# Optimization experiments

Hardware: AMD Instinct MI355X
Metric: run time of the kernel (lower is better)

Reference implementation:

```python
import jax, jax.numpy as jnp
import numpy as np

D_MODEL = 512
N_HEADS = 8
DH = D_MODEL // N_HEADS


def _split_heads(x, h):
    B, L, D = x.shape
    return x.reshape(B, L, h, D // h).transpose(0, 2, 1, 3)  # [B,h,L,Dh]


def setup_inputs() -> dict:
    key = jax.random.key(0)
    ks = jax.random.split(key, 10)
    B, La, Lb, Lc = 4, 256, 256, 32
    s = 1.0 / np.sqrt(D_MODEL)
    return {
        "Q_in": jax.random.normal(ks[0], (B, La, D_MODEL), jnp.float32),
        "K_in": jax.random.normal(ks[1], (B, Lb, D_MODEL), jnp.float32),
        "V_in": jax.random.normal(ks[2], (B, Lb, D_MODEL), jnp.float32),
        "C_tokens": jax.random.normal(ks[3], (B, Lc, D_MODEL), jnp.float32),
        "Wq": jax.random.normal(ks[4], (D_MODEL, D_MODEL), jnp.float32) * s,
        "bq": jnp.zeros((D_MODEL,), jnp.float32),
        "Wk": jax.random.normal(ks[5], (D_MODEL, D_MODEL), jnp.float32) * s,
        "bk": jnp.zeros((D_MODEL,), jnp.float32),
        "Wv": jax.random.normal(ks[6], (D_MODEL, D_MODEL), jnp.float32) * s,
        "bv": jnp.zeros((D_MODEL,), jnp.float32),
    }


def reference(Q_in, K_in, V_in, C_tokens, Wq, bq, Wk, bk, Wv, bv):
    B, La, D = Q_in.shape
    Lb = K_in.shape[1]
    Lc = C_tokens.shape[1]
    h = N_HEADS
    # torch Linear: y = x @ W.T + b
    Q = _split_heads(Q_in @ Wq.T + bq, h)        # [B,h,La,Dh]
    K = _split_heads(K_in @ Wk.T + bk, h)        # [B,h,Lb,Dh]
    V = _split_heads(V_in @ Wv.T + bv, h)        # [B,h,Lb,Dh]
    C = _split_heads(C_tokens, h)                # [B,h,Lc,Dh]
    # tri-linear TSDP score: [B,h,La,Lb,Lc]
    scores = jnp.einsum('bhqd,bhkd,bhcd->bhqkc', Q, K, C) / np.sqrt(DH)
    scores = scores.reshape(B, h, La, Lb * Lc)
    attn = jax.nn.softmax(scores, axis=-1)       # no mask path; all_masked trivially False
    attn5 = attn.reshape(B, h, La, Lb, Lc)
    # cv_mode='mul': VC[k,c,d] = V[k,d]*C[c,d]; fuse contraction, never materialize VC
    out = jnp.einsum('bhqkc,bhkd,bhcd->bhqd', attn5, V, C)
    out = out.transpose(0, 2, 1, 3).reshape(B, La, D)
    return (out, attn)
```

## Files before the change

### kernel.cpp

```cpp
#include <hip/hip_runtime.h>
#include <hip/hip_bf16.h>
#include <math.h>

#define D_MODEL 512
#define NH 8
#define DH 64
#define LA 256
#define LB 256
#define LC 32
#define BATCH 4
#define KC_TOT 8192
#define XN (BATCH * LA * D_MODEL)
#define WN (D_MODEL * D_MODEL)

typedef float f32x4 __attribute__((ext_vector_type(4)));
typedef _Float16 f16x8 __attribute__((ext_vector_type(8)));
typedef _Float16 f16x4 __attribute__((ext_vector_type(4)));
typedef unsigned int u32;

#if __has_builtin(__builtin_amdgcn_exp2f)
#define EXP2(x) __builtin_amdgcn_exp2f(x)
#else
#define EXP2(x) exp2f(x)
#endif
#define SCLOG2E 0.18033688011118324f

#define MFMA16F(a, b, c) __builtin_amdgcn_mfma_f32_16x16x32_f16(a, b, c, 0, 0, 0)

static __device__ __forceinline__ u32 pkrtz(float x, float y) {
  auto t = __builtin_amdgcn_cvt_pkrtz(x, y);
  u32 r; __builtin_memcpy(&r, &t, 4);
  return r;
}

__global__ __launch_bounds__(256) void cvt_kernel(
    const float* __restrict__ X0, const float* __restrict__ X1,
    const float* __restrict__ X2, const float* __restrict__ W0,
    const float* __restrict__ W1, const float* __restrict__ W2,
    _Float16* __restrict__ dst)
{
  const int t = blockIdx.y;
  const float* src;
  size_t n, off;
  switch (t) {
    case 0: src = X0; n = XN; off = 0; break;
    case 1: src = X1; n = XN; off = (size_t)XN; break;
    case 2: src = X2; n = XN; off = 2 * (size_t)XN; break;
    case 3: src = W0; n = WN; off = 3 * (size_t)XN; break;
    case 4: src = W1; n = WN; off = 3 * (size_t)XN + WN; break;
    default: src = W2; n = WN; off = 3 * (size_t)XN + 2 * (size_t)WN; break;
  }
  const size_t i = (size_t)blockIdx.x * 2048 + threadIdx.x * 8;
  if (i >= n) return;
  float4 a = *(const float4*)(src + i);
  float4 b = *(const float4*)(src + i + 4);
  f16x8 r;
  r[0] = (_Float16)a.x; r[1] = (_Float16)a.y; r[2] = (_Float16)a.z; r[3] = (_Float16)a.w;
  r[4] = (_Float16)b.x; r[5] = (_Float16)b.y; r[6] = (_Float16)b.z; r[7] = (_Float16)b.w;
  *(f16x8*)(dst + off + i) = r;
}

__global__ __launch_bounds__(256) void proj_mfma(
    const _Float16* __restrict__ XWh,
    const float* __restrict__ bq, const float* __restrict__ bk,
    const float* __restrict__ bv,
    _Float16* __restrict__ Qp, _Float16* __restrict__ Kp,
    _Float16* __restrict__ Vp)
{
  const int z = blockIdx.z;
  const _Float16* X = XWh + (size_t)z * XN;
  const _Float16* W = XWh + 3 * (size_t)XN + (size_t)z * WN;
  const float* bias = (z == 0) ? bq : (z == 1) ? bk : bv;
  _Float16* Y = (z == 0) ? Qp : (z == 1) ? Kp : Vp;

  const int tid = threadIdx.x;
  const int lane = tid & 63;
  const int w = tid >> 6;
  const int l16 = lane & 15;
  const int lg = lane >> 4;

  const int n0 = blockIdx.x * 64;
  const int m0 = blockIdx.y * 64;
  const int m = m0 + w * 16 + l16;

  f32x4 acc[4] = {};
  const _Float16* xrow = X + (size_t)m * D_MODEL;
  const _Float16* wbase = W + (size_t)(n0 + l16) * D_MODEL;

#pragma unroll 4
  for (int ks = 0; ks < 16; ++ks) {
    f16x8 bf = *(const f16x8*)(xrow + ks * 32 + lg * 8);
#pragma unroll
    for (int ai = 0; ai < 4; ++ai) {
      f16x8 af = *(const f16x8*)(wbase + (size_t)(ai * 16) * D_MODEL + ks * 32 + lg * 8);
      acc[ai] = MFMA16F(af, bf, acc[ai]);
    }
  }
#pragma unroll
  for (int ai = 0; ai < 4; ++ai) {
    float4 b4 = *(const float4*)&bias[n0 + ai * 16 + lg * 4];
    f16x4 r;
    r[0] = (_Float16)(acc[ai][0] + b4.x);
    r[1] = (_Float16)(acc[ai][1] + b4.y);
    r[2] = (_Float16)(acc[ai][2] + b4.z);
    r[3] = (_Float16)(acc[ai][3] + b4.w);
    *(f16x4*)&Y[(size_t)m * D_MODEL + n0 + ai * 16 + lg * 4] = r;
  }
}


__global__ __launch_bounds__(256) void k1_rowsum(
    const _Float16* __restrict__ Qp, const _Float16* __restrict__ Kp,
    const float* __restrict__ Ct, float* __restrict__ ws_rs)
{
  __shared__ __align__(16) _Float16 K_lds[128][DH];
  __shared__ __align__(16) _Float16 C_lds[LC][DH + 8];
  __shared__ float red[4][16];

  const int tid = threadIdx.x;
  const int lane = tid & 63;
  const int w = tid >> 6;
  const int l16 = lane & 15;
  const int lg = lane >> 4;

  const int tile = blockIdx.x >> 1;
  const int half = blockIdx.x & 1;
  const int bh = tile >> 4;
  const int qt = tile & 15;
  const int b = bh >> 3;
  const int h = bh & 7;

  const _Float16* Kb = Kp + (size_t)b * LB * D_MODEL + h * DH;
  const float* Cb = Ct + (size_t)b * LC * D_MODEL + h * DH;

  for (int i = tid; i < 128 * DH / 8; i += 256) {
    const int k = i >> 3, dg = (i & 7) * 8;
    *(f16x8*)&K_lds[k][dg] = *(const f16x8*)(Kb + (size_t)(half * 128 + k) * D_MODEL + dg);
  }
  for (int i = tid; i < LC * DH; i += 256) {
    const int c = i >> 6, d = i & 63;
    C_lds[c][d] = (_Float16)Cb[(size_t)c * D_MODEL + d];
  }

  f16x8 qf[2];
  {
    const _Float16* Qb = Qp + (size_t)(b * LA + qt * 16) * D_MODEL + h * DH;
#pragma unroll
    for (int kh = 0; kh < 2; ++kh)
      qf[kh] = *(const f16x8*)(Qb + (size_t)l16 * D_MODEL + kh * 32 + lg * 8);
  }
  __syncthreads();

  float rs = 0.f;
#pragma unroll 2
  for (int ch = 0; ch < 32; ++ch) {
    const int krow = w * 32 + ch;
    f32x4 s0 = {0.f, 0.f, 0.f, 0.f}, s1 = {0.f, 0.f, 0.f, 0.f};
#pragma unroll
    for (int kh = 0; kh < 2; ++kh) {
      f16x8 kv = *(const f16x8*)&K_lds[krow][kh * 32 + lg * 8];
      f16x8 c0 = *(const f16x8*)&C_lds[l16][kh * 32 + lg * 8];
      f16x8 c1 = *(const f16x8*)&C_lds[16 + l16][kh * 32 + lg * 8];
      s0 = MFMA16F(kv * c0, qf[kh], s0);
      s1 = MFMA16F(kv * c1, qf[kh], s1);
    }
#pragma unroll
    for (int r = 0; r < 4; ++r)
      rs += EXP2(s0[r] * SCLOG2E) + EXP2(s1[r] * SCLOG2E);
  }
  rs += __shfl_xor(rs, 16);
  rs += __shfl_xor(rs, 32);
  if (lane < 16) red[w][lane] = rs;
  __syncthreads();
  if (tid < 16)
    ws_rs[tile * 32 + half * 16 + tid] = red[0][tid] + red[1][tid] + red[2][tid] + red[3][tid];
}

__global__ __launch_bounds__(256) void k2_emit(
    const _Float16* __restrict__ Qp, const _Float16* __restrict__ Kp,
    const _Float16* __restrict__ Vp, const float* __restrict__ Ct,
    const float* __restrict__ ws_rs, float* __restrict__ attn,
    float* __restrict__ ws_out)
{
  __shared__ __align__(16) _Float16 K_lds[128][DH];
  __shared__ __align__(16) _Float16 C_lds[LC][DH + 8];
  __shared__ __align__(16) _Float16 CT_lds[DH][LC + 8];

  const int tid = threadIdx.x;
  const int lane = tid & 63;
  const int w = tid >> 6;
  const int l16 = lane & 15;
  const int lg = lane >> 4;

  const int tile = blockIdx.x >> 1;
  const int half = blockIdx.x & 1;
  const int bh = tile >> 4;
  const int qt = tile & 15;
  const int b = bh >> 3;
  const int h = bh & 7;

  const _Float16* Kb = Kp + (size_t)b * LB * D_MODEL + h * DH;
  const _Float16* Vb = Vp + (size_t)b * LB * D_MODEL + h * DH;
  const float* Cb = Ct + (size_t)b * LC * D_MODEL + h * DH;

  for (int i = tid; i < 128 * DH / 8; i += 256) {
    const int k = i >> 3, dg = (i & 7) * 8;
    *(f16x8*)&K_lds[k][dg] = *(const f16x8*)(Kb + (size_t)(half * 128 + k) * D_MODEL + dg);
  }
  for (int i = tid; i < LC * DH; i += 256) {
    const int c = i >> 6, d = i & 63;
    _Float16 v = (_Float16)Cb[(size_t)c * D_MODEL + d];
    C_lds[c][d] = v;
    CT_lds[d][c] = v;
  }

  f16x8 qf[2];
  {
    const _Float16* Qb = Qp + (size_t)(b * LA + qt * 16) * D_MODEL + h * DH;
#pragma unroll
    for (int kh = 0; kh < 2; ++kh)
      qf[kh] = *(const f16x8*)(Qb + (size_t)l16 * D_MODEL + kh * 32 + lg * 8);
  }
  const float inv = 1.f / (ws_rs[tile * 32 + l16] + ws_rs[tile * 32 + 16 + l16]);
  __syncthreads();

  f32x4 oacc[4] = {};
  float* arow = attn + (size_t)(bh * LA + qt * 16 + l16) * KC_TOT + half * 4096 + w * 1024;
  const int s1i = l16 + ((lg & 1) << 5);
  const int s2i = s1i + 16;

#pragma unroll 2
  for (int ch = 0; ch < 32; ++ch) {
    const int krow = w * 32 + ch;
    f32x4 s0 = {0.f, 0.f, 0.f, 0.f}, s1 = {0.f, 0.f, 0.f, 0.f};
#pragma unroll
    for (int kh = 0; kh < 2; ++kh) {
      f16x8 kv = *(const f16x8*)&K_lds[krow][kh * 32 + lg * 8];
      f16x8 c0 = *(const f16x8*)&C_lds[l16][kh * 32 + lg * 8];
      f16x8 c1 = *(const f16x8*)&C_lds[16 + l16][kh * 32 + lg * 8];
      s0 = MFMA16F(kv * c0, qf[kh], s0);
      s1 = MFMA16F(kv * c1, qf[kh], s1);
    }
    f32x4 p0, p1;
#pragma unroll
    for (int r = 0; r < 4; ++r) {
      p0[r] = EXP2(s0[r] * SCLOG2E) * inv;
      p1[r] = EXP2(s1[r] * SCLOG2E) * inv;
    }
    *(f32x4*)(arow + ch * 32 + lg * 4) = p0;
    *(f32x4*)(arow + ch * 32 + 16 + lg * 4) = p1;

    const u32 a0 = pkrtz(p0[0], p0[1]), a1 = pkrtz(p0[2], p0[3]);
    const u32 b0 = pkrtz(p1[0], p1[1]), b1 = pkrtz(p1[2], p1[3]);
    const u32 sa0 = (u32)__shfl((int)a0, s1i), sb0 = (u32)__shfl((int)b0, s1i);
    const u32 sa1 = (u32)__shfl((int)a1, s1i), sb1 = (u32)__shfl((int)b1, s1i);
    const u32 ta0 = (u32)__shfl((int)a0, s2i), tb0 = (u32)__shfl((int)b0, s2i);
    const u32 ta1 = (u32)__shfl((int)a1, s2i), tb1 = (u32)__shfl((int)b1, s2i);
    u32 bw[4];
    bw[0] = (lg < 2) ? sa0 : sb0;
    bw[1] = (lg < 2) ? sa1 : sb1;
    bw[2] = (lg < 2) ? ta0 : tb0;
    bw[3] = (lg < 2) ? ta1 : tb1;
    f16x8 bf; __builtin_memcpy(&bf, bw, 16);

    const _Float16* vrow = Vb + (size_t)(half * 128 + krow) * D_MODEL;
#pragma unroll
    for (int dt = 0; dt < 4; ++dt) {
      const _Float16 vv = vrow[dt * 16 + l16];
      f16x8 ct8 = *(const f16x8*)&CT_lds[dt * 16 + l16][lg * 8];
      oacc[dt] = MFMA16F(ct8 * vv, bf, oacc[dt]);
    }
  }

  __syncthreads();
  float* obuf = (float*)&K_lds[0][0];
#pragma unroll
  for (int dt = 0; dt < 4; ++dt)
#pragma unroll
    for (int r = 0; r < 4; ++r)
      obuf[w * 1024 + l16 * 64 + dt * 16 + lg * 4 + r] = oacc[dt][r];
  __syncthreads();
  for (int e = tid; e < 1024; e += 256)
    ws_out[(size_t)(tile * 2 + half) * 1024 + e] =
        obuf[e] + obuf[1024 + e] + obuf[2048 + e] + obuf[3072 + e];
}

__global__ __launch_bounds__(256) void k3_reduce(
    const float* __restrict__ ws_out, float* __restrict__ out)
{
  const int o = blockIdx.x * 256 + threadIdx.x;
  const int col = o & 511;
  const int row = o >> 9;
  const int b = row >> 8;
  const int q = row & 255;
  const int h = col >> 6;
  const int d = col & 63;
  const int tile = (b * 8 + h) * 16 + (q >> 4);
  const float* p = ws_out + (size_t)tile * 2048 + (q & 15) * 64 + d;
  out[o] = p[0] + p[1024];
}

extern "C" void kernel_launch(void* const* d_in, const int* in_sizes, int n_in,
                              void* d_out, int out_size, void* d_ws, size_t ws_size,
                              hipStream_t stream) {
  const float* Q_in     = (const float*)d_in[0];
  const float* K_in     = (const float*)d_in[1];
  const float* V_in     = (const float*)d_in[2];
  const float* C_tokens = (const float*)d_in[3];
  const float* Wq       = (const float*)d_in[4];
  const float* bq       = (const float*)d_in[5];
  const float* Wk       = (const float*)d_in[6];
  const float* bk       = (const float*)d_in[7];
  const float* Wv       = (const float*)d_in[8];
  const float* bv       = (const float*)d_in[9];

  float* outp  = (float*)d_out;
  float* attnp = outp + (size_t)BATCH * LA * D_MODEL;

  _Float16* Qp  = (_Float16*)d_ws;
  _Float16* Kp  = Qp + (size_t)XN;
  _Float16* Vp  = Kp + (size_t)XN;
  _Float16* XWh = Vp + (size_t)XN;
  float* wsf    = (float*)(XWh + 3 * (size_t)XN + 3 * (size_t)WN);
  float* ws_rs  = wsf;
  float* ws_out = wsf + 512 * 32;

  cvt_kernel<<<dim3(256, 6), 256, 0, stream>>>(Q_in, K_in, V_in, Wq, Wk, Wv, XWh);
  proj_mfma<<<dim3(8, 16, 3), 256, 0, stream>>>(XWh, bq, bk, bv, Qp, Kp, Vp);
  k1_rowsum<<<1024, 256, 0, stream>>>(Qp, Kp, C_tokens, ws_rs);
  k2_emit<<<1024, 256, 0, stream>>>(Qp, Kp, Vp, C_tokens, ws_rs, attnp, ws_out);
  k3_reduce<<<(BATCH * LA * D_MODEL) / 256, 256, 0, stream>>>(ws_out, outp);
}
```

Before: 114.6 us.

## Fuse rowsum, emit and reduce kernels into one 512-thread attention kernel

Merges the separate row-sum pass, the attention-emit pass and the final reduction kernel into one kernel. Each block now handles a full 16-query tile across all 256 keys with 8 waves, keeping the softmax denominator in LDS and writing the output directly. This removes two kernel launches, the workspace round-trips for row sums and partial outputs, and the duplicated K/C staging across half-blocks. In exchange the grid is halved to 512 blocks with larger LDS use per block, which may reduce occupancy and latency hiding.

```diff
diff --git a/kernel.cpp b/kernel.cpp
--- a/kernel.cpp
+++ b/kernel.cpp
@@ -108,14 +108,16 @@
   }
 }
 
-
-__global__ __launch_bounds__(256) void k1_rowsum(
+__global__ __launch_bounds__(512) void attn_fused(
     const _Float16* __restrict__ Qp, const _Float16* __restrict__ Kp,
-    const float* __restrict__ Ct, float* __restrict__ ws_rs)
+    const _Float16* __restrict__ Vp, const float* __restrict__ Ct,
+    float* __restrict__ attn, float* __restrict__ out)
 {
-  __shared__ __align__(16) _Float16 K_lds[128][DH];
+  __shared__ __align__(16) _Float16 K_lds[LB][DH];
   __shared__ __align__(16) _Float16 C_lds[LC][DH + 8];
-  __shared__ float red[4][16];
+  __shared__ __align__(16) _Float16 CT_lds[DH][LC + 8];
+  __shared__ float red_lds[8][16];
+  __shared__ float inv_lds[16];
 
   const int tid = threadIdx.x;
   const int lane = tid & 63;
@@ -123,23 +125,25 @@
   const int l16 = lane & 15;
   const int lg = lane >> 4;
 
-  const int tile = blockIdx.x >> 1;
-  const int half = blockIdx.x & 1;
+  const int tile = blockIdx.x;
   const int bh = tile >> 4;
   const int qt = tile & 15;
   const int b = bh >> 3;
   const int h = bh & 7;
 
   const _Float16* Kb = Kp + (size_t)b * LB * D_MODEL + h * DH;
+  const _Float16* Vb = Vp + (size_t)b * LB * D_MODEL + h * DH;
   const float* Cb = Ct + (size_t)b * LC * D_MODEL + h * DH;
 
-  for (int i = tid; i < 128 * DH / 8; i += 256) {
+  for (int i = tid; i < LB * DH / 8; i += 512) {
     const int k = i >> 3, dg = (i & 7) * 8;
-    *(f16x8*)&K_lds[k][dg] = *(const f16x8*)(Kb + (size_t)(half * 128 + k) * D_MODEL + dg);
-  }
-  for (int i = tid; i < LC * DH; i += 256) {
+    *(f16x8*)&K_lds[k][dg] = *(const f16x8*)(Kb + (size_t)k * D_MODEL + dg);
+  }
+  for (int i = tid; i < LC * DH; i += 512) {
     const int c = i >> 6, d = i & 63;
-    C_lds[c][d] = (_Float16)Cb[(size_t)c * D_MODEL + d];
+    _Float16 v = (_Float16)Cb[(size_t)c * D_MODEL + d];
+    C_lds[c][d] = v;
+    CT_lds[d][c] = v;
   }
 
   f16x8 qf[2];
@@ -170,62 +174,19 @@
   }
   rs += __shfl_xor(rs, 16);
   rs += __shfl_xor(rs, 32);
-  if (lane < 16) red[w][lane] = rs;
-  __syncthreads();
-  if (tid < 16)
-    ws_rs[tile * 32 + half * 16 + tid] = red[0][tid] + red[1][tid] + red[2][tid] + red[3][tid];
-}
-
-__global__ __launch_bounds__(256) void k2_emit(
-    const _Float16* __restrict__ Qp, const _Float16* __restrict__ Kp,
-    const _Float16* __restrict__ Vp, const float* __restrict__ Ct,
-    const float* __restrict__ ws_rs, float* __restrict__ attn,
-    float* __restrict__ ws_out)
-{
-  __shared__ __align__(16) _Float16 K_lds[128][DH];
-  __shared__ __align__(16) _Float16 C_lds[LC][DH + 8];
-  __shared__ __align__(16) _Float16 CT_lds[DH][LC + 8];
-
-  const int tid = threadIdx.x;
-  const int lane = tid & 63;
-  const int w = tid >> 6;
-  const int l16 = lane & 15;
-  const int lg = lane >> 4;
-
-  const int tile = blockIdx.x >> 1;
-  const int half = blockIdx.x & 1;
-  const int bh = tile >> 4;
-  const int qt = tile & 15;
-  const int b = bh >> 3;
-  const int h = bh & 7;
-
-  const _Float16* Kb = Kp + (size_t)b * LB * D_MODEL + h * DH;
-  const _Float16* Vb = Vp + (size_t)b * LB * D_MODEL + h * DH;
-  const float* Cb = Ct + (size_t)b * LC * D_MODEL + h * DH;
-
-  for (int i = tid; i < 128 * DH / 8; i += 256) {
-    const int k = i >> 3, dg = (i & 7) * 8;
-    *(f16x8*)&K_lds[k][dg] = *(const f16x8*)(Kb + (size_t)(half * 128 + k) * D_MODEL + dg);
-  }
-  for (int i = tid; i < LC * DH; i += 256) {
-    const int c = i >> 6, d = i & 63;
-    _Float16 v = (_Float16)Cb[(size_t)c * D_MODEL + d];
-    C_lds[c][d] = v;
-    CT_lds[d][c] = v;
-  }
-
-  f16x8 qf[2];
-  {
-    const _Float16* Qb = Qp + (size_t)(b * LA + qt * 16) * D_MODEL + h * DH;
-#pragma unroll
-    for (int kh = 0; kh < 2; ++kh)
-      qf[kh] = *(const f16x8*)(Qb + (size_t)l16 * D_MODEL + kh * 32 + lg * 8);
-  }
-  const float inv = 1.f / (ws_rs[tile * 32 + l16] + ws_rs[tile * 32 + 16 + l16]);
-  __syncthreads();
+  if (lane < 16) red_lds[w][lane] = rs;
+  __syncthreads();
+  if (tid < 16) {
+    float t = 0.f;
+#pragma unroll
+    for (int ww = 0; ww < 8; ++ww) t += red_lds[ww][tid];
+    inv_lds[tid] = 1.f / t;
+  }
+  __syncthreads();
+  const float inv = inv_lds[l16];
 
   f32x4 oacc[4] = {};
-  float* arow = attn + (size_t)(bh * LA + qt * 16 + l16) * KC_TOT + half * 4096 + w * 1024;
+  float* arow = attn + (size_t)(bh * LA + qt * 16 + l16) * KC_TOT + w * 1024;
   const int s1i = l16 + ((lg & 1) << 5);
   const int s2i = s1i + 16;
 
@@ -263,7 +224,7 @@
     bw[3] = (lg < 2) ? ta1 : tb1;
     f16x8 bf; __builtin_memcpy(&bf, bw, 16);
 
-    const _Float16* vrow = Vb + (size_t)(half * 128 + krow) * D_MODEL;
+    const _Float16* vrow = Vb + (size_t)krow * D_MODEL;
 #pragma unroll
     for (int dt = 0; dt < 4; ++dt) {
       const _Float16 vv = vrow[dt * 16 + l16];
@@ -280,24 +241,13 @@
     for (int r = 0; r < 4; ++r)
       obuf[w * 1024 + l16 * 64 + dt * 16 + lg * 4 + r] = oacc[dt][r];
   __syncthreads();
-  for (int e = tid; e < 1024; e += 256)
-    ws_out[(size_t)(tile * 2 + half) * 1024 + e] =
-        obuf[e] + obuf[1024 + e] + obuf[2048 + e] + obuf[3072 + e];
-}
-
-__global__ __launch_bounds__(256) void k3_reduce(
-    const float* __restrict__ ws_out, float* __restrict__ out)
-{
-  const int o = blockIdx.x * 256 + threadIdx.x;
-  const int col = o & 511;
-  const int row = o >> 9;
-  const int b = row >> 8;
-  const int q = row & 255;
-  const int h = col >> 6;
-  const int d = col & 63;
-  const int tile = (b * 8 + h) * 16 + (q >> 4);
-  const float* p = ws_out + (size_t)tile * 2048 + (q & 15) * 64 + d;
-  out[o] = p[0] + p[1024];
+  for (int e = tid; e < 1024; e += 512) {
+    float t = 0.f;
+#pragma unroll
+    for (int ww = 0; ww < 8; ++ww) t += obuf[ww * 1024 + e];
+    const int qq = e >> 6, d = e & 63;
+    out[(size_t)(b * LA + qt * 16 + qq) * D_MODEL + h * DH + d] = t;
+  }
 }
 
 extern "C" void kernel_launch(void* const* d_in, const int* in_sizes, int n_in,
@@ -321,13 +271,8 @@
   _Float16* Kp  = Qp + (size_t)XN;
   _Float16* Vp  = Kp + (size_t)XN;
   _Float16* XWh = Vp + (size_t)XN;
-  float* wsf    = (float*)(XWh + 3 * (size_t)XN + 3 * (size_t)WN);
-  float* ws_rs  = wsf;
-  float* ws_out = wsf + 512 * 32;
 
   cvt_kernel<<<dim3(256, 6), 256, 0, stream>>>(Q_in, K_in, V_in, Wq, Wk, Wv, XWh);
   proj_mfma<<<dim3(8, 16, 3), 256, 0, stream>>>(XWh, bq, bk, bv, Qp, Kp, Vp);
-  k1_rowsum<<<1024, 256, 0, stream>>>(Qp, Kp, C_tokens, ws_rs);
-  k2_emit<<<1024, 256, 0, stream>>>(Qp, Kp, Vp, C_tokens, ws_rs, attnp, ws_out);
-  k3_reduce<<<(BATCH * LA * D_MODEL) / 256, 256, 0, stream>>>(ws_out, outp);
-}
+  attn_fused<<<512, 512, 0, stream>>>(Qp, Kp, Vp, C_tokens, attnp, outp);
+}
```

Result: faster. 103.4 us (-9.8%).
